# Kernel optimization log

Hardware: AMD Instinct MI355X
Metric: run time of the kernel (lower is better)

Reference implementation:

```python
import jax, jax.numpy as jnp
import numpy as np

DIM = 512
T = 65536


def setup_inputs() -> dict:
    key = jax.random.key(0)
    k1, = jax.random.split(key, 1)
    z_rest = jax.random.normal(k1, (T, DIM), dtype=jnp.float32)
    # var_vbl = inv_softplus(sqrt(var_init)) with var_init=1.0 -> log(expm1(1.0))
    var_vbl = jnp.full((DIM,), float(np.log(np.expm1(1.0))), dtype=jnp.float32)
    # corr_vbl = inv_sigmoid(0.1) = log(0.1) - log(0.9)
    corr_vbl = jnp.full((DIM,), float(np.log(0.1) - np.log(0.9)), dtype=jnp.float32)
    prior_mu = jnp.zeros((DIM,), dtype=jnp.float32)
    return {"z_rest": z_rest, "var_vbl": var_vbl, "corr_vbl": corr_vbl, "prior_mu": prior_mu}


def reference(z_rest, var_vbl, corr_vbl, prior_mu):
    # init_train_lkd with z_context=None, starting from fresh state (sample_size=0).
    prior_var = jnp.square(jax.nn.softplus(var_vbl))          # [D]
    prior_cov = jax.nn.sigmoid(corr_vbl) * prior_var          # [D]
    two_pi = 2.0 * jnp.pi

    def step(carry, xs):
        mu, var, lkd = carry
        z, t = xs  # z: [D], t: scalar step index (== sample_size - 1 after increment)
        lkd = lkd + jnp.sum(-0.5 * jnp.log(two_pi * var)
                            - jnp.square(z - mu) / (2.0 * var))
        dd = prior_cov / (prior_var + prior_cov * t)
        mu = (1.0 - dd) * mu + z * dd
        var = (1.0 - dd) * var + (prior_var - prior_cov) * dd
        return (mu, var, lkd), None

    ts = jnp.arange(z_rest.shape[0], dtype=z_rest.dtype)
    init = (prior_mu.astype(z_rest.dtype), prior_var, jnp.zeros((), z_rest.dtype))
    (_, _, lkd), _ = jax.lax.scan(step, init, (z_rest, ts))
    return lkd
```

## Files before the change

### kernel.cpp

```cpp
#include <hip/hip_runtime.h>
#include <math.h>


#define DIM    512
#define TT     65536
#define CHUNKS 2048
#define ROWS   32
#define GROUPS 64
#define CPG    32

#define TWO_PI 6.283185307179586

__global__ __launch_bounds__(128) void k1_colsum(const float* __restrict__ z,
                                                 float* __restrict__ sums) {
    const int chunk = blockIdx.x;
    const int t = threadIdx.x;
    const float4* zp = reinterpret_cast<const float4*>(z)
                       + (size_t)chunk * ROWS * (DIM / 4) + t;
    float sx = 0.f, sy = 0.f, sz = 0.f, sw = 0.f;
#pragma unroll 8
    for (int r = 0; r < ROWS; ++r) {
        float4 v = zp[(size_t)r * (DIM / 4)];
        sx += v.x; sy += v.y; sz += v.z; sw += v.w;
    }
    float4* sp = reinterpret_cast<float4*>(sums) + (size_t)chunk * (DIM / 4) + t;
    *sp = make_float4(sx, sy, sz, sw);
}

__global__ __launch_bounds__(512) void k2a_scan(float* __restrict__ sums,
                                                float* __restrict__ gsums) {
    const int g = blockIdx.x;
    const int d = threadIdx.x;
    float run = 0.f;
#pragma unroll 8
    for (int i = 0; i < CPG; ++i) {
        const size_t idx = (size_t)(g * CPG + i) * DIM + d;
        float t = sums[idx];
        sums[idx] = run;
        run += t;
    }
    gsums[(size_t)g * DIM + d] = run;
}

__global__ __launch_bounds__(512) void k2b_scan(float* __restrict__ gsums,
                                                const float* __restrict__ var_vbl,
                                                const float* __restrict__ corr_vbl,
                                                float* __restrict__ out) {
    const int d = threadIdx.x;
    float run = 0.f;
#pragma unroll 8
    for (int g = 0; g < GROUPS; ++g) {
        float t = gsums[(size_t)g * DIM + d];
        gsums[(size_t)g * DIM + d] = run;
        run += t;
    }
    double sp = log1p(exp((double)var_vbl[d]));
    double v = sp * sp;
    double cc = v / (1.0 + exp(-(double)corr_vbl[d]));
    double vmc = v - cc;
    double Dlast = v + cc * (double)(TT - 1);
    double Ld = -0.5 * ((double)TT * (log(TWO_PI) + log(vmc)) + log(Dlast / vmc));
    __shared__ double red[512];
    red[d] = Ld;
    __syncthreads();
    for (int s = 256; s > 0; s >>= 1) {
        if (d < s) red[d] += red[d + s];
        __syncthreads();
    }
    if (d == 0) out[0] = (float)red[0];
}

__global__ __launch_bounds__(128) void k3_main(const float* __restrict__ z,
                                               const float* __restrict__ sums,
                                               const float* __restrict__ gsums,
                                               const float* __restrict__ var_vbl,
                                               const float* __restrict__ corr_vbl,
                                               const float* __restrict__ prior_mu,
                                               float* __restrict__ out) {
    const int chunk = blockIdx.x;
    const int tid = threadIdx.x;
    const int d0 = tid * 4;
    const int g = chunk / CPG;
    const float t0m1 = (float)(chunk * ROWS) - 1.0f;

    float vv[4], cc[4], k0[4], kq[4], Z[4], Dprev[4], invDprev[4];
#pragma unroll
    for (int j = 0; j < 4; ++j) {
        const int d = d0 + j;
        float spv = log1pf(expf(var_vbl[d]));
        float v = spv * spv;
        float c = v / (1.0f + expf(-corr_vbl[d]));
        float vmc = v - c;
        vv[j] = v;
        cc[j] = c;
        k0[j] = vmc * prior_mu[d];
        kq[j] = 0.5f / vmc;
        Z[j] = sums[(size_t)chunk * DIM + d] + gsums[(size_t)g * DIM + d];
        Dprev[j] = fmaf(c, t0m1, v);
        invDprev[j] = __builtin_amdgcn_rcpf(Dprev[j]);
    }

    const float4* zp = reinterpret_cast<const float4*>(z)
                       + (size_t)chunk * ROWS * (DIM / 4) + tid;
    float acc = 0.f;
    float tf = t0m1 + 1.0f;
#pragma unroll 4
    for (int r = 0; r < ROWS; ++r) {
        float4 zv = zp[(size_t)r * (DIM / 4)];
        float zz[4] = {zv.x, zv.y, zv.z, zv.w};
#pragma unroll
        for (int j = 0; j < 4; ++j) {
            float Dt = fmaf(cc[j], tf, vv[j]);
            float invDt = __builtin_amdgcn_rcpf(Dt);
            float mu = fmaf(cc[j], Z[j], k0[j]) * invDprev[j];
            float e = zz[j] - mu;
            acc = fmaf(e * e * Dprev[j] * invDt, kq[j], acc);
            Z[j] += zz[j];
            Dprev[j] = Dt;
            invDprev[j] = invDt;
        }
        tf += 1.0f;
    }

    for (int off = 32; off > 0; off >>= 1) acc += __shfl_down(acc, off, 64);
    __shared__ float wsred[2];
    const int lane = tid & 63, w = tid >> 6;
    if (lane == 0) wsred[w] = acc;
    __syncthreads();
    if (tid == 0) atomicAdd(out, -(wsred[0] + wsred[1]));
}

extern "C" void kernel_launch(void* const* d_in, const int* in_sizes, int n_in,
                              void* d_out, int out_size, void* d_ws, size_t ws_size,
                              hipStream_t stream) {
    const float* z = (const float*)d_in[0];
    const float* var_vbl = (const float*)d_in[1];
    const float* corr_vbl = (const float*)d_in[2];
    const float* prior_mu = (const float*)d_in[3];
    float* out = (float*)d_out;
    float* sums = (float*)d_ws;
    float* gsums = sums + (size_t)CHUNKS * DIM;

    k1_colsum<<<CHUNKS, 128, 0, stream>>>(z, sums);
    k2a_scan<<<GROUPS, 512, 0, stream>>>(sums, gsums);
    k2b_scan<<<1, 512, 0, stream>>>(gsums, var_vbl, corr_vbl, out);
    k3_main<<<CHUNKS, 128, 0, stream>>>(z, sums, gsums, var_vbl, corr_vbl,
                                        prior_mu, out);
}
```

Baseline: 242.5 us.

## Fuse four scan kernels into one cooperative kernel with grid syncs

Merges the column-sum, two scan levels, constant-term computation and main likelihood pass into a single cooperative kernel separated by grid-wide syncs. It also halves the block count and doubles rows per block so all blocks can be co-resident. The aim is to remove launch overhead between the four kernels and let the second pass over z hit in cache. The cost is three grid syncs and only 64 or 1 blocks doing work during the middle scan phases.

```diff
diff --git a/kernel.cpp b/kernel.cpp
--- a/kernel.cpp
+++ b/kernel.cpp
@@ -1,133 +1,142 @@
 #include <hip/hip_runtime.h>
+#include <hip/hip_cooperative_groups.h>
 #include <math.h>
+
+namespace cg = cooperative_groups;
 
 
 #define DIM    512
 #define TT     65536
-#define CHUNKS 2048
-#define ROWS   32
+#define BLOCKS 1024
+#define ROWS   64
 #define GROUPS 64
-#define CPG    32
-
+#define CPG    16
 #define TWO_PI 6.283185307179586
 
-__global__ __launch_bounds__(128) void k1_colsum(const float* __restrict__ z,
-                                                 float* __restrict__ sums) {
-    const int chunk = blockIdx.x;
-    const int t = threadIdx.x;
-    const float4* zp = reinterpret_cast<const float4*>(z)
-                       + (size_t)chunk * ROWS * (DIM / 4) + t;
-    float sx = 0.f, sy = 0.f, sz = 0.f, sw = 0.f;
-#pragma unroll 8
-    for (int r = 0; r < ROWS; ++r) {
-        float4 v = zp[(size_t)r * (DIM / 4)];
-        sx += v.x; sy += v.y; sz += v.z; sw += v.w;
-    }
-    float4* sp = reinterpret_cast<float4*>(sums) + (size_t)chunk * (DIM / 4) + t;
-    *sp = make_float4(sx, sy, sz, sw);
-}
-
-__global__ __launch_bounds__(512) void k2a_scan(float* __restrict__ sums,
-                                                float* __restrict__ gsums) {
-    const int g = blockIdx.x;
-    const int d = threadIdx.x;
-    float run = 0.f;
-#pragma unroll 8
-    for (int i = 0; i < CPG; ++i) {
-        const size_t idx = (size_t)(g * CPG + i) * DIM + d;
-        float t = sums[idx];
-        sums[idx] = run;
-        run += t;
-    }
-    gsums[(size_t)g * DIM + d] = run;
-}
-
-__global__ __launch_bounds__(512) void k2b_scan(float* __restrict__ gsums,
-                                                const float* __restrict__ var_vbl,
-                                                const float* __restrict__ corr_vbl,
-                                                float* __restrict__ out) {
-    const int d = threadIdx.x;
-    float run = 0.f;
-#pragma unroll 8
-    for (int g = 0; g < GROUPS; ++g) {
-        float t = gsums[(size_t)g * DIM + d];
-        gsums[(size_t)g * DIM + d] = run;
-        run += t;
-    }
-    double sp = log1p(exp((double)var_vbl[d]));
-    double v = sp * sp;
-    double cc = v / (1.0 + exp(-(double)corr_vbl[d]));
-    double vmc = v - cc;
-    double Dlast = v + cc * (double)(TT - 1);
-    double Ld = -0.5 * ((double)TT * (log(TWO_PI) + log(vmc)) + log(Dlast / vmc));
-    __shared__ double red[512];
-    red[d] = Ld;
-    __syncthreads();
-    for (int s = 256; s > 0; s >>= 1) {
-        if (d < s) red[d] += red[d + s];
-        __syncthreads();
-    }
-    if (d == 0) out[0] = (float)red[0];
-}
-
-__global__ __launch_bounds__(128) void k3_main(const float* __restrict__ z,
-                                               const float* __restrict__ sums,
-                                               const float* __restrict__ gsums,
-                                               const float* __restrict__ var_vbl,
-                                               const float* __restrict__ corr_vbl,
-                                               const float* __restrict__ prior_mu,
-                                               float* __restrict__ out) {
+__global__ __launch_bounds__(128, 2) void fused_all(
+        const float* __restrict__ z,
+        const float* __restrict__ var_vbl,
+        const float* __restrict__ corr_vbl,
+        const float* __restrict__ prior_mu,
+        float* __restrict__ out,
+        float* __restrict__ sums,
+        float* __restrict__ gsums) {
+    cg::grid_group grid = cg::this_grid();
     const int chunk = blockIdx.x;
     const int tid = threadIdx.x;
-    const int d0 = tid * 4;
-    const int g = chunk / CPG;
-    const float t0m1 = (float)(chunk * ROWS) - 1.0f;
 
-    float vv[4], cc[4], k0[4], kq[4], Z[4], Dprev[4], invDprev[4];
+    __shared__ double red[128];
+
+    {
+        const float4* zp = reinterpret_cast<const float4*>(z)
+                           + (size_t)chunk * ROWS * (DIM / 4) + tid;
+        float4 s = make_float4(0.f, 0.f, 0.f, 0.f);
+#pragma unroll 8
+        for (int r = 0; r < ROWS; ++r) {
+            float4 v = zp[(size_t)r * (DIM / 4)];
+            s.x += v.x; s.y += v.y; s.z += v.z; s.w += v.w;
+        }
+        reinterpret_cast<float4*>(sums)[(size_t)chunk * (DIM / 4) + tid] = s;
+    }
+    grid.sync();
+
+    if (chunk < GROUPS) {
+        const int g = chunk;
+        float4 run = make_float4(0.f, 0.f, 0.f, 0.f);
 #pragma unroll
-    for (int j = 0; j < 4; ++j) {
-        const int d = d0 + j;
-        float spv = log1pf(expf(var_vbl[d]));
-        float v = spv * spv;
-        float c = v / (1.0f + expf(-corr_vbl[d]));
-        float vmc = v - c;
-        vv[j] = v;
-        cc[j] = c;
-        k0[j] = vmc * prior_mu[d];
-        kq[j] = 0.5f / vmc;
-        Z[j] = sums[(size_t)chunk * DIM + d] + gsums[(size_t)g * DIM + d];
-        Dprev[j] = fmaf(c, t0m1, v);
-        invDprev[j] = __builtin_amdgcn_rcpf(Dprev[j]);
+        for (int i = 0; i < CPG; ++i) {
+            float4* p = reinterpret_cast<float4*>(sums)
+                        + (size_t)(g * CPG + i) * (DIM / 4) + tid;
+            float4 t = *p;
+            *p = run;
+            run.x += t.x; run.y += t.y; run.z += t.z; run.w += t.w;
+        }
+        reinterpret_cast<float4*>(gsums)[(size_t)g * (DIM / 4) + tid] = run;
     }
+    grid.sync();
 
-    const float4* zp = reinterpret_cast<const float4*>(z)
-                       + (size_t)chunk * ROWS * (DIM / 4) + tid;
-    float acc = 0.f;
-    float tf = t0m1 + 1.0f;
-#pragma unroll 4
-    for (int r = 0; r < ROWS; ++r) {
-        float4 zv = zp[(size_t)r * (DIM / 4)];
-        float zz[4] = {zv.x, zv.y, zv.z, zv.w};
+    if (chunk == 0) {
+        float4 run = make_float4(0.f, 0.f, 0.f, 0.f);
+#pragma unroll 8
+        for (int g = 0; g < GROUPS; ++g) {
+            float4* p = reinterpret_cast<float4*>(gsums)
+                        + (size_t)g * (DIM / 4) + tid;
+            float4 t = *p;
+            *p = run;
+            run.x += t.x; run.y += t.y; run.z += t.z; run.w += t.w;
+        }
+        double Lsum = 0.0;
 #pragma unroll
         for (int j = 0; j < 4; ++j) {
-            float Dt = fmaf(cc[j], tf, vv[j]);
-            float invDt = __builtin_amdgcn_rcpf(Dt);
-            float mu = fmaf(cc[j], Z[j], k0[j]) * invDprev[j];
-            float e = zz[j] - mu;
-            acc = fmaf(e * e * Dprev[j] * invDt, kq[j], acc);
-            Z[j] += zz[j];
-            Dprev[j] = Dt;
-            invDprev[j] = invDt;
+            const int d = tid * 4 + j;
+            double sp = log1p(exp((double)var_vbl[d]));
+            double v = sp * sp;
+            double c = v / (1.0 + exp(-(double)corr_vbl[d]));
+            double vmc = v - c;
+            double Dlast = v + c * (double)(TT - 1);
+            Lsum += -0.5 * ((double)TT * (log(TWO_PI) + log(vmc)) + log(Dlast / vmc));
         }
-        tf += 1.0f;
+        red[tid] = Lsum;
+        __syncthreads();
+        for (int s = 64; s > 0; s >>= 1) {
+            if (tid < s) red[tid] += red[tid + s];
+            __syncthreads();
+        }
+        if (tid == 0) out[0] = (float)red[0];
     }
+    grid.sync();
 
-    for (int off = 32; off > 0; off >>= 1) acc += __shfl_down(acc, off, 64);
-    __shared__ float wsred[2];
-    const int lane = tid & 63, w = tid >> 6;
-    if (lane == 0) wsred[w] = acc;
-    __syncthreads();
-    if (tid == 0) atomicAdd(out, -(wsred[0] + wsred[1]));
+    {
+        const int d0 = tid * 4;
+        const int g = chunk / CPG;
+        const float t0m1 = (float)(chunk * ROWS) - 1.0f;
+
+        float vv[4], cc[4], k0[4], kq[4], Z[4], Dprev[4], invDprev[4];
+#pragma unroll
+        for (int j = 0; j < 4; ++j) {
+            const int d = d0 + j;
+            float spv = log1pf(expf(var_vbl[d]));
+            float v = spv * spv;
+            float c = v / (1.0f + expf(-corr_vbl[d]));
+            float vmc = v - c;
+            vv[j] = v;
+            cc[j] = c;
+            k0[j] = vmc * prior_mu[d];
+            kq[j] = 0.5f / vmc;
+            Z[j] = sums[(size_t)chunk * DIM + d] + gsums[(size_t)g * DIM + d];
+            Dprev[j] = fmaf(c, t0m1, v);
+            invDprev[j] = __builtin_amdgcn_rcpf(Dprev[j]);
+        }
+
+        const float4* zp = reinterpret_cast<const float4*>(z)
+                           + (size_t)chunk * ROWS * (DIM / 4) + tid;
+        float acc = 0.f;
+        float tf = t0m1 + 1.0f;
+#pragma unroll 4
+        for (int r = 0; r < ROWS; ++r) {
+            float4 zv = zp[(size_t)r * (DIM / 4)];
+            float zz[4] = {zv.x, zv.y, zv.z, zv.w};
+#pragma unroll
+            for (int j = 0; j < 4; ++j) {
+                float Dt = fmaf(cc[j], tf, vv[j]);
+                float invDt = __builtin_amdgcn_rcpf(Dt);
+                float mu = fmaf(cc[j], Z[j], k0[j]) * invDprev[j];
+                float e = zz[j] - mu;
+                acc = fmaf(e * e * Dprev[j] * invDt, kq[j], acc);
+                Z[j] += zz[j];
+                Dprev[j] = Dt;
+                invDprev[j] = invDt;
+            }
+            tf += 1.0f;
+        }
+
+        for (int off = 32; off > 0; off >>= 1) acc += __shfl_down(acc, off, 64);
+        __shared__ float wsred[2];
+        const int lane = tid & 63, w = tid >> 6;
+        if (lane == 0) wsred[w] = acc;
+        __syncthreads();
+        if (tid == 0) atomicAdd(out, -(wsred[0] + wsred[1]));
+    }
 }
 
 extern "C" void kernel_launch(void* const* d_in, const int* in_sizes, int n_in,
@@ -139,11 +148,10 @@
     const float* prior_mu = (const float*)d_in[3];
     float* out = (float*)d_out;
     float* sums = (float*)d_ws;
-    float* gsums = sums + (size_t)CHUNKS * DIM;
+    float* gsums = sums + (size_t)BLOCKS * DIM;
 
-    k1_colsum<<<CHUNKS, 128, 0, stream>>>(z, sums);
-    k2a_scan<<<GROUPS, 512, 0, stream>>>(sums, gsums);
-    k2b_scan<<<1, 512, 0, stream>>>(gsums, var_vbl, corr_vbl, out);
-    k3_main<<<CHUNKS, 128, 0, stream>>>(z, sums, gsums, var_vbl, corr_vbl,
-                                        prior_mu, out);
+    void* args[] = {(void*)&z, (void*)&var_vbl, (void*)&corr_vbl, (void*)&prior_mu,
+                    (void*)&out, (void*)&sums, (void*)&gsums};
+    hipLaunchCooperativeKernel((const void*)fused_all, dim3(BLOCKS), dim3(128),
+                               args, 0, stream);
 }
```

Result: slower. 548.9 us (+126.3%).

## Replace two-pass prefix scan with single pass using quadratic-in-offset partial sums

Applied to the files above, without the earlier changes.

Each chunk now computes its local likelihood terms as a quadratic in the unknown prefix column-sum offset, storing A, B, C coefficients and local sums. A second kernel combines them once prefix sums are known. This removes the separate column-sum pass and a scan kernel, so z is read once instead of twice. In exchange it writes and reads four workspace planes. The expansion A - 2ZB + Z²C in float32 risks cancellation error with large prefix sums.

```diff
diff --git a/kernel.cpp b/kernel.cpp
--- a/kernel.cpp
+++ b/kernel.cpp
@@ -4,86 +4,27 @@
 
 #define DIM    512
 #define TT     65536
-#define CHUNKS 2048
-#define ROWS   32
-#define GROUPS 64
-#define CPG    32
-
+#define CHUNKS 1024
+#define ROWS   64
+#define K2B    64
+#define CPB    16
 #define TWO_PI 6.283185307179586
 
-__global__ __launch_bounds__(128) void k1_colsum(const float* __restrict__ z,
-                                                 float* __restrict__ sums) {
-    const int chunk = blockIdx.x;
-    const int t = threadIdx.x;
-    const float4* zp = reinterpret_cast<const float4*>(z)
-                       + (size_t)chunk * ROWS * (DIM / 4) + t;
-    float sx = 0.f, sy = 0.f, sz = 0.f, sw = 0.f;
-#pragma unroll 8
-    for (int r = 0; r < ROWS; ++r) {
-        float4 v = zp[(size_t)r * (DIM / 4)];
-        sx += v.x; sy += v.y; sz += v.z; sw += v.w;
-    }
-    float4* sp = reinterpret_cast<float4*>(sums) + (size_t)chunk * (DIM / 4) + t;
-    *sp = make_float4(sx, sy, sz, sw);
-}
-
-__global__ __launch_bounds__(512) void k2a_scan(float* __restrict__ sums,
-                                                float* __restrict__ gsums) {
-    const int g = blockIdx.x;
-    const int d = threadIdx.x;
-    float run = 0.f;
-#pragma unroll 8
-    for (int i = 0; i < CPG; ++i) {
-        const size_t idx = (size_t)(g * CPG + i) * DIM + d;
-        float t = sums[idx];
-        sums[idx] = run;
-        run += t;
-    }
-    gsums[(size_t)g * DIM + d] = run;
-}
-
-__global__ __launch_bounds__(512) void k2b_scan(float* __restrict__ gsums,
-                                                const float* __restrict__ var_vbl,
-                                                const float* __restrict__ corr_vbl,
-                                                float* __restrict__ out) {
-    const int d = threadIdx.x;
-    float run = 0.f;
-#pragma unroll 8
-    for (int g = 0; g < GROUPS; ++g) {
-        float t = gsums[(size_t)g * DIM + d];
-        gsums[(size_t)g * DIM + d] = run;
-        run += t;
-    }
-    double sp = log1p(exp((double)var_vbl[d]));
-    double v = sp * sp;
-    double cc = v / (1.0 + exp(-(double)corr_vbl[d]));
-    double vmc = v - cc;
-    double Dlast = v + cc * (double)(TT - 1);
-    double Ld = -0.5 * ((double)TT * (log(TWO_PI) + log(vmc)) + log(Dlast / vmc));
-    __shared__ double red[512];
-    red[d] = Ld;
-    __syncthreads();
-    for (int s = 256; s > 0; s >>= 1) {
-        if (d < s) red[d] += red[d + s];
-        __syncthreads();
-    }
-    if (d == 0) out[0] = (float)red[0];
-}
-
-__global__ __launch_bounds__(128) void k3_main(const float* __restrict__ z,
-                                               const float* __restrict__ sums,
-                                               const float* __restrict__ gsums,
+__global__ __launch_bounds__(128) void k1_pass(const float* __restrict__ z,
                                                const float* __restrict__ var_vbl,
                                                const float* __restrict__ corr_vbl,
                                                const float* __restrict__ prior_mu,
+                                               float* __restrict__ ws,
                                                float* __restrict__ out) {
     const int chunk = blockIdx.x;
     const int tid = threadIdx.x;
     const int d0 = tid * 4;
-    const int g = chunk / CPG;
     const float t0m1 = (float)(chunk * ROWS) - 1.0f;
 
-    float vv[4], cc[4], k0[4], kq[4], Z[4], Dprev[4], invDprev[4];
+    if (chunk == 0 && tid == 0) out[0] = 0.0f;
+
+    float vv[4], cc[4], k0[4], kq[4], zeta[4], Dprev[4], invDprev[4];
+    float A[4], B[4], C[4];
 #pragma unroll
     for (int j = 0; j < 4; ++j) {
         const int d = d0 + j;
@@ -91,18 +32,17 @@
         float v = spv * spv;
         float c = v / (1.0f + expf(-corr_vbl[d]));
         float vmc = v - c;
-        vv[j] = v;
-        cc[j] = c;
+        vv[j] = v; cc[j] = c;
         k0[j] = vmc * prior_mu[d];
         kq[j] = 0.5f / vmc;
-        Z[j] = sums[(size_t)chunk * DIM + d] + gsums[(size_t)g * DIM + d];
+        zeta[j] = 0.f;
         Dprev[j] = fmaf(c, t0m1, v);
         invDprev[j] = __builtin_amdgcn_rcpf(Dprev[j]);
+        A[j] = 0.f; B[j] = 0.f; C[j] = 0.f;
     }
 
     const float4* zp = reinterpret_cast<const float4*>(z)
                        + (size_t)chunk * ROWS * (DIM / 4) + tid;
-    float acc = 0.f;
     float tf = t0m1 + 1.0f;
 #pragma unroll 4
     for (int r = 0; r < ROWS; ++r) {
@@ -112,22 +52,77 @@
         for (int j = 0; j < 4; ++j) {
             float Dt = fmaf(cc[j], tf, vv[j]);
             float invDt = __builtin_amdgcn_rcpf(Dt);
-            float mu = fmaf(cc[j], Z[j], k0[j]) * invDprev[j];
-            float e = zz[j] - mu;
-            acc = fmaf(e * e * Dprev[j] * invDt, kq[j], acc);
-            Z[j] += zz[j];
+            float u = zz[j] - fmaf(cc[j], zeta[j], k0[j]) * invDprev[j];
+            float w = Dprev[j] * invDt * kq[j];
+            float p = cc[j] * invDprev[j];
+            float wu = w * u;
+            float wp = w * p;
+            A[j] = fmaf(wu, u, A[j]);
+            B[j] = fmaf(wu, p, B[j]);
+            C[j] = fmaf(wp, p, C[j]);
+            zeta[j] += zz[j];
             Dprev[j] = Dt;
             invDprev[j] = invDt;
         }
         tf += 1.0f;
     }
 
-    for (int off = 32; off > 0; off >>= 1) acc += __shfl_down(acc, off, 64);
-    __shared__ float wsred[2];
-    const int lane = tid & 63, w = tid >> 6;
-    if (lane == 0) wsred[w] = acc;
+    const size_t base = (size_t)chunk * (DIM / 4) + tid;
+    const size_t plane = (size_t)CHUNKS * (DIM / 4);
+    float4* w4 = reinterpret_cast<float4*>(ws);
+    w4[base]             = make_float4(zeta[0], zeta[1], zeta[2], zeta[3]);
+    w4[base + plane]     = make_float4(A[0], A[1], A[2], A[3]);
+    w4[base + 2 * plane] = make_float4(B[0], B[1], B[2], B[3]);
+    w4[base + 3 * plane] = make_float4(C[0], C[1], C[2], C[3]);
+}
+
+__global__ __launch_bounds__(512) void k2_combine(const float* __restrict__ ws,
+                                                  const float* __restrict__ var_vbl,
+                                                  const float* __restrict__ corr_vbl,
+                                                  float* __restrict__ out) {
+    const int g = blockIdx.x;
+    const int d = threadIdx.x;
+    const float* cs = ws;
+    const float* Ap = ws + (size_t)CHUNKS * DIM;
+    const float* Bp = Ap + (size_t)CHUNKS * DIM;
+    const float* Cp = Bp + (size_t)CHUNKS * DIM;
+
+    const int lim = g * CPB;
+    float z0 = 0.f, z1 = 0.f, z2 = 0.f, z3 = 0.f;
+    for (int i = 0; i + 3 < lim; i += 4) {
+        z0 += cs[(size_t)i * DIM + d];
+        z1 += cs[(size_t)(i + 1) * DIM + d];
+        z2 += cs[(size_t)(i + 2) * DIM + d];
+        z3 += cs[(size_t)(i + 3) * DIM + d];
+    }
+    float Zc = (z0 + z1) + (z2 + z3);
+
+    float q = 0.f;
+#pragma unroll
+    for (int i = 0; i < CPB; ++i) {
+        const size_t idx = (size_t)(g * CPB + i) * DIM + d;
+        q += Ap[idx] - 2.0f * Zc * Bp[idx] + Zc * Zc * Cp[idx];
+        Zc += cs[idx];
+    }
+
+    double contrib = -(double)q;
+    if (g == 0) {
+        double sp = log1p(exp((double)var_vbl[d]));
+        double v = sp * sp;
+        double c = v / (1.0 + exp(-(double)corr_vbl[d]));
+        double vmc = v - c;
+        double Dlast = v + c * (double)(TT - 1);
+        contrib += -0.5 * ((double)TT * (log(TWO_PI) + log(vmc)) + log(Dlast / vmc));
+    }
+
+    __shared__ double red[512];
+    red[d] = contrib;
     __syncthreads();
-    if (tid == 0) atomicAdd(out, -(wsred[0] + wsred[1]));
+    for (int s = 256; s > 0; s >>= 1) {
+        if (d < s) red[d] += red[d + s];
+        __syncthreads();
+    }
+    if (d == 0) atomicAdd(out, (float)red[0]);
 }
 
 extern "C" void kernel_launch(void* const* d_in, const int* in_sizes, int n_in,
@@ -138,12 +133,8 @@
     const float* corr_vbl = (const float*)d_in[2];
     const float* prior_mu = (const float*)d_in[3];
     float* out = (float*)d_out;
-    float* sums = (float*)d_ws;
-    float* gsums = sums + (size_t)CHUNKS * DIM;
+    float* ws = (float*)d_ws;
 
-    k1_colsum<<<CHUNKS, 128, 0, stream>>>(z, sums);
-    k2a_scan<<<GROUPS, 512, 0, stream>>>(sums, gsums);
-    k2b_scan<<<1, 512, 0, stream>>>(gsums, var_vbl, corr_vbl, out);
-    k3_main<<<CHUNKS, 128, 0, stream>>>(z, sums, gsums, var_vbl, corr_vbl,
-                                        prior_mu, out);
+    k1_pass<<<CHUNKS, 128, 0, stream>>>(z, var_vbl, corr_vbl, prior_mu, ws, out);
+    k2_combine<<<K2B, 512, 0, stream>>>(ws, var_vbl, corr_vbl, out);
 }
```

New measurement: 262.0 us. +8.0%, slower.
